# Kernel optimization log

Measured on AMD Instinct MI355X. Metric: run time of the kernel, lower is better.

Reference implementation:

```python
import jax, jax.numpy as jnp
import numpy as np
from jax import lax

B, N, S, C_IN, C_OUT = 4, 16384, 4096, 256, 256


def setup_inputs() -> dict:
    key = jax.random.key(0)
    k1, k2, k3, k4 = jax.random.split(key, 4)
    xyz1 = jax.random.normal(k1, (B, 3, N), dtype=jnp.float32)
    xyz2 = jax.random.normal(k2, (B, 3, S), dtype=jnp.float32)
    points2 = jax.random.normal(k3, (B, C_IN, S), dtype=jnp.float32)
    W = jax.random.normal(k4, (C_OUT, C_IN), dtype=jnp.float32) * (1.0 / np.sqrt(C_IN))
    b = jnp.zeros((C_OUT,), dtype=jnp.float32)
    return {"xyz1": xyz1, "xyz2": xyz2, "points2": points2, "W": W, "b": b}


def reference(xyz1, xyz2, points2, W, b):
    # channel-first -> channel-last
    p1 = jnp.transpose(xyz1, (0, 2, 1))        # [B, N, 3]
    p2 = jnp.transpose(xyz2, (0, 2, 1))        # [B, S, 3]
    f2 = jnp.transpose(points2, (0, 2, 1))     # [B, S, C]
    Bn, Nn, _ = p1.shape
    Cn = f2.shape[-1]
    # squared pairwise distances [B, N, S]
    d = (-2.0 * jnp.einsum('bnc,bsc->bns', p1, p2)
         + jnp.sum(p1 * p1, axis=-1)[:, :, None]
         + jnp.sum(p2 * p2, axis=-1)[:, None, :])
    # 3 nearest neighbors (smallest distances) -- equivalent to sort + slice :3
    neg_d3, idx = lax.top_k(-d, 3)             # [B, N, 3]
    d3 = -neg_d3
    recip = 1.0 / (d3 + 1e-8)
    weight = recip / jnp.sum(recip, axis=-1, keepdims=True)   # [B, N, 3]
    # gather neighbor features: [B, N, 3, C]
    gathered = jnp.take_along_axis(
        f2, idx.reshape(Bn, Nn * 3)[..., None], axis=1
    ).reshape(Bn, Nn, 3, Cn)
    interp = jnp.sum(gathered * weight[..., None], axis=2)    # [B, N, C]
    # Conv1d(kernel=1) == per-point linear: [B, C_out, N]
    out = jnp.einsum('bnc,oc->bon', interp, W) + b[None, :, None]
    return out
```

## Files before the change

### kernel.cpp

```cpp
#include <hip/hip_runtime.h>

#define BB 4
#define NN 16384
#define SS 4096
#define CIN 256
#define COUT 256

#define SC 8
#define SCS (SS / SC)
#define SUBS 16
#define SUBL 256
#define KNNB ((NN / 512) * SC * BB)
#define GEMMB ((COUT / 64) * (SS / 64) * BB)

typedef float v2f __attribute__((ext_vector_type(2)));
typedef float v4f __attribute__((ext_vector_type(4)));

__device__ __forceinline__ unsigned short f2bf(float f) {
    unsigned u = __float_as_uint(f);
    u += 0x7FFF + ((u >> 16) & 1);
    return (unsigned short)(u >> 16);
}
__device__ __forceinline__ float bf2f(unsigned short h) {
    return __uint_as_float((unsigned)h << 16);
}

__device__ __forceinline__ void insert_vi(float e, int gi,
                                          float& k0, float& k1, float& k2,
                                          int& i0, int& i1, int& i2) {
    bool c0 = e < k0, c1 = e < k1, c2 = e < k2;
    float n0 = fminf(e, k0);
    float n1 = __builtin_amdgcn_fmed3f(e, k0, k1);
    float n2 = __builtin_amdgcn_fmed3f(e, k1, k2);
    int t1 = c0 ? i0 : gi;
    int t2 = c1 ? i1 : gi;
    i0 = c0 ? gi : i0;
    i1 = c1 ? t1 : i1;
    i2 = c2 ? t2 : i2;
    k0 = n0; k1 = n1; k2 = n2;
}

#define E2_FROM(p_xy, p_zw, XX, YY, ZZ, e2)                                    \
    do {                                                                       \
        asm("v_pk_fma_f32 %0, %1, %2, %3 op_sel:[0,0,1] op_sel_hi:[0,1,1]"     \
            : "=v"(e2) : "v"(p_zw), "v"(ZZ), "v"(p_zw));                       \
        asm("v_pk_fma_f32 %0, %1, %2, %0 op_sel:[1,0,0] op_sel_hi:[1,1,1]"     \
            : "+v"(e2) : "v"(p_xy), "v"(YY));                                  \
        asm("v_pk_fma_f32 %0, %1, %2, %0 op_sel:[0,0,0] op_sel_hi:[0,1,1]"     \
            : "+v"(e2) : "v"(p_xy), "v"(XX));                                  \
    } while (0)

#define PK_LO(acc, ap, bw)                                                     \
    asm("v_pk_fma_f32 %0, %1, %2, %0 op_sel:[0,0,0] op_sel_hi:[0,1,1]"         \
        : "+v"(acc) : "v"(ap), "v"(bw))
#define PK_HI(acc, ap, bw)                                                     \
    asm("v_pk_fma_f32 %0, %1, %2, %0 op_sel:[1,0,0] op_sel_hi:[1,1,1]"         \
        : "+v"(acc) : "v"(ap), "v"(bw))

__device__ __forceinline__ void knn_phase(int id, int t, float* smem,
                                          const float* __restrict__ xyz1,
                                          const float* __restrict__ xyz2,
                                          float* __restrict__ pv) {
    int nb = id & 31;
    int ch = (id >> 5) & 7;
    int b  = id >> 8;
    int s0 = ch * SCS;

    float4* smv = (float4*)smem;
    const float* x2 = xyz2 + (size_t)b * 3 * SS;
    for (int i = t; i < SCS; i += 256) {
        float px = x2[s0 + i];
        float py = x2[SS + s0 + i];
        float pz = x2[2 * SS + s0 + i];
        smv[i] = make_float4(px, py, pz, fmaf(px, px, fmaf(py, py, pz * pz)));
    }
    __syncthreads();

    int n0  = nb * 512 + t;
    int n1q = n0 + 256;
    const float* xb = xyz1 + (size_t)b * 3 * NN;
    float ax = xb[n0],  ay = xb[NN + n0],  az = xb[2 * NN + n0];
    float bx = xb[n1q], by = xb[NN + n1q], bz = xb[2 * NN + n1q];
    v2f XX = {-2.0f * ax, -2.0f * bx};
    v2f YY = {-2.0f * ay, -2.0f * by};
    v2f ZZ = {-2.0f * az, -2.0f * bz};

#pragma unroll
    for (int half = 0; half < 2; ++half) {
        float A0 = 1e30f, A1 = 1e30f, A2 = 1e30f;
        float B0 = 1e30f, B1 = 1e30f, B2 = 1e30f;
        int sb = half * SUBL;
#pragma unroll 8
        for (int s = sb; s < sb + SUBL; ++s) {
            v4f p = *(const v4f*)(smem + 4 * s);
            v2f pxy = __builtin_shufflevector(p, p, 0, 1);
            v2f pzw = __builtin_shufflevector(p, p, 2, 3);
            v2f e2;
            E2_FROM(pxy, pzw, XX, YY, ZZ, e2);
            float nA1 = __builtin_amdgcn_fmed3f(e2.x, A0, A1);
            float nA2 = __builtin_amdgcn_fmed3f(e2.x, A1, A2);
            A0 = fminf(A0, e2.x); A1 = nA1; A2 = nA2;
            float nB1 = __builtin_amdgcn_fmed3f(e2.y, B0, B1);
            float nB2 = __builtin_amdgcn_fmed3f(e2.y, B1, B2);
            B0 = fminf(B0, e2.y); B1 = nB1; B2 = nB2;
        }
        int sub = ch * 2 + half;
        size_t base = (size_t)(sub * BB + b) * 3;
        pv[(base + 0) * NN + n0]  = A0;
        pv[(base + 1) * NN + n0]  = A1;
        pv[(base + 2) * NN + n0]  = A2;
        pv[(base + 0) * NN + n1q] = B0;
        pv[(base + 1) * NN + n1q] = B1;
        pv[(base + 2) * NN + n1q] = B2;
    }
}

__device__ __forceinline__ void gemm_phase(int g, int t, float* smem,
                                           const float* __restrict__ P,
                                           const float* __restrict__ W,
                                           const float* __restrict__ bias,
                                           unsigned short* __restrict__ Gh) {
    int o0 = (g & 3) * 64;
    int s0 = ((g >> 2) & 63) * 64;
    int b  = g >> 8;
    float* sP = smem;
    float* sW = smem + 1024;
    int i = t & 15;
    int j = t >> 4;

    v2f acc2[4][2];
#pragma unroll
    for (int p = 0; p < 4; ++p) {
        acc2[p][0] = (v2f){0.f, 0.f};
        acc2[p][1] = (v2f){0.f, 0.f};
    }

    const float* Pb = P + (size_t)b * CIN * SS;

    for (int c0 = 0; c0 < CIN; c0 += 16) {
        __syncthreads();
        {
            int col = t & 63;
            int r0r = t >> 6;
#pragma unroll
            for (int r = 0; r < 4; ++r) {
                int row = r0r + r * 4;
                sP[row * 64 + col] = Pb[(size_t)(c0 + row) * SS + s0 + col];
            }
        }
        {
            int cc = t & 15;
            int obase = t >> 4;
#pragma unroll
            for (int r = 0; r < 4; ++r) {
                int oo = obase + 16 * r;
                sW[cc * 68 + oo] = W[(size_t)(o0 + oo) * CIN + c0 + cc];
            }
        }
        __syncthreads();

#pragma unroll
        for (int cc = 0; cc < 16; ++cc) {
            v4f a  = *(const v4f*)&sP[cc * 64 + i * 4];
            v4f bv = *(const v4f*)&sW[cc * 68 + j * 4];
            v2f a01 = __builtin_shufflevector(a, a, 0, 1);
            v2f a23 = __builtin_shufflevector(a, a, 2, 3);
            v2f b01 = __builtin_shufflevector(bv, bv, 0, 1);
            v2f b23 = __builtin_shufflevector(bv, bv, 2, 3);
            PK_LO(acc2[0][0], a01, b01); PK_LO(acc2[0][1], a01, b23);
            PK_HI(acc2[1][0], a01, b01); PK_HI(acc2[1][1], a01, b23);
            PK_LO(acc2[2][0], a23, b01); PK_LO(acc2[2][1], a23, b23);
            PK_HI(acc2[3][0], a23, b01); PK_HI(acc2[3][1], a23, b23);
        }
    }

    float b0 = bias[o0 + j * 4 + 0];
    float b1 = bias[o0 + j * 4 + 1];
    float b2 = bias[o0 + j * 4 + 2];
    float b3 = bias[o0 + j * 4 + 3];
#pragma unroll
    for (int p = 0; p < 4; ++p) {
        ushort4 v;
        v.x = f2bf(acc2[p][0].x + b0);
        v.y = f2bf(acc2[p][0].y + b1);
        v.z = f2bf(acc2[p][1].x + b2);
        v.w = f2bf(acc2[p][1].y + b3);
        size_t off = ((size_t)b * SS + s0 + i * 4 + p) * COUT + o0 + j * 4;
        *(ushort4*)&Gh[off] = v;
    }
}

__global__ __launch_bounds__(256) void k_fused(const float* __restrict__ xyz1,
                                               const float* __restrict__ xyz2,
                                               const float* __restrict__ P,
                                               const float* __restrict__ W,
                                               const float* __restrict__ bias,
                                               unsigned short* __restrict__ Gh,
                                               float* __restrict__ pv) {
    __shared__ float smem[2112];
    int bid = blockIdx.x;
    int t   = threadIdx.x;

    if (bid < KNNB) {
        knn_phase(bid, t, smem, xyz1, xyz2, pv);
    } else {
        gemm_phase(bid - KNNB, t, smem, P, W, bias, Gh);
    }
}

__global__ __launch_bounds__(256) void k_resolve(const float* __restrict__ pv,
                                                 const float* __restrict__ xyz1,
                                                 const float* __restrict__ xyz2,
                                                 float4* __restrict__ wi4,
                                                 int4* __restrict__ gi4) {
    __shared__ float4 cand[4096];
    int b    = blockIdx.x >> 6;
    int nblk = blockIdx.x & 63;
    int t    = threadIdx.x;

    const float* x2 = xyz2 + (size_t)b * 3 * SS;
    for (int i = t; i < SS; i += 256) {
        int sub = i >> 8, s = i & 255;
        float px = x2[i];
        float py = x2[SS + i];
        float pz = x2[2 * SS + i];
        cand[sub * SUBL + (s ^ (sub & 7))] =
            make_float4(px, py, pz, fmaf(px, px, fmaf(py, py, pz * pz)));
    }
    __syncthreads();

    int n = nblk * 256 + t;

    float v0 = 1e30f, v1 = 1e30f, v2v = 1e30f;
#pragma unroll 4
    for (int sub = 0; sub < SUBS; ++sub) {
        size_t base = (size_t)(sub * BB + b) * 3;
#pragma unroll
        for (int j = 0; j < 3; ++j) {
            float a  = pv[(base + j) * NN + n];
            float t1 = __builtin_amdgcn_fmed3f(a, v0, v1);
            float t2 = __builtin_amdgcn_fmed3f(a, v1, v2v);
            v0 = fminf(v0, a); v1 = t1; v2v = t2;
        }
    }

    int l0 = 0, l1 = 0, l2 = 0, l3 = 0, cnt = 0;
#pragma unroll 4
    for (int sub = 0; sub < SUBS; ++sub) {
        float a0 = pv[(size_t)(sub * BB + b) * 3 * NN + n];
        if (a0 <= v2v) {
            if      (cnt == 0) l0 = sub;
            else if (cnt == 1) l1 = sub;
            else if (cnt == 2) l2 = sub;
            else if (cnt == 3) l3 = sub;
            ++cnt;
        }
    }

    const float* xb = xyz1 + (size_t)b * 3 * NN;
    float qx = xb[n], qy = xb[NN + n], qz = xb[2 * NN + n];
    float xm2 = -2.0f * qx, ym2 = -2.0f * qy, zm2 = -2.0f * qz;
    float nrm = fmaf(qx, qx, fmaf(qy, qy, qz * qz));

    float k0 = 1e30f, k1 = 1e30f, k2 = 1e30f;
    int   i0 = 0,     i1 = 0,     i2 = 0;
    bool ovf  = (cnt > 4);
    int  kmax = ovf ? SUBS : cnt;
    for (int k = 0; k < kmax; ++k) {
        int sub = ovf ? k : (k == 0 ? l0 : (k == 1 ? l1 : (k == 2 ? l2 : l3)));
        int xr = sub & 7;
        int sb = sub * SUBL;
#pragma unroll 8
        for (int s = 0; s < SUBL; ++s) {
            float4 p = cand[sb + (s ^ xr)];
            float e = fmaf(p.x, xm2, fmaf(p.y, ym2, fmaf(p.z, zm2, p.w)));
            insert_vi(e, sb + s, k0, k1, k2, i0, i1, i2);
        }
    }

    float d0 = k0 + nrm, d1 = k1 + nrm, d2 = k2 + nrm;
    float r0 = 1.0f / (d0 + 1e-8f);
    float r1 = 1.0f / (d1 + 1e-8f);
    float r2 = 1.0f / (d2 + 1e-8f);
    float inv = 1.0f / (r0 + r1 + r2);
    size_t q = (size_t)b * NN + n;
    wi4[q] = make_float4(r0 * inv, r1 * inv, r2 * inv, 0.f);
    gi4[q] = make_int4(i0, i1, i2, 0);
}

__global__ __launch_bounds__(256) void k_out(const unsigned short* __restrict__ Gh,
                                             const float4* __restrict__ wi4,
                                             const int4* __restrict__ gi4,
                                             float* __restrict__ out) {
    __shared__ float  tile[64 * 68];
    __shared__ float4 swv[64];
    __shared__ int4   siv[64];
    int bid  = blockIdx.x;
    int x    = bid & 7;
    int b    = x >> 1;
    int local = (bid >> 3) + (x & 1) * 512;
    int nb   = local & 255;
    int oc   = local >> 8;
    int n0   = nb * 64;
    int o0   = oc * 64;
    int t    = threadIdx.x;
    int wave = t >> 6;
    int lane = t & 63;
    int qg   = lane >> 4;
    int c16  = lane & 15;

    if (t < 64) {
        size_t q = (size_t)b * NN + n0 + t;
        swv[t] = wi4[q];
        siv[t] = gi4[q];
    }
    __syncthreads();

    const unsigned short* Gb = Gh + (size_t)b * SS * COUT;

#pragma unroll
    for (int pass = 0; pass < 4; ++pass) {
        int q = pass * 16 + wave * 4 + qg;
        float4 wv = swv[q];
        int4   iv = siv[q];
        int co = o0 + c16 * 4;
        ushort4 a0 = *(const ushort4*)(Gb + (size_t)iv.x * COUT + co);
        ushort4 a1 = *(const ushort4*)(Gb + (size_t)iv.y * COUT + co);
        ushort4 a2 = *(const ushort4*)(Gb + (size_t)iv.z * COUT + co);
        float4 v;
        v.x = fmaf(wv.x, bf2f(a0.x), fmaf(wv.y, bf2f(a1.x), wv.z * bf2f(a2.x)));
        v.y = fmaf(wv.x, bf2f(a0.y), fmaf(wv.y, bf2f(a1.y), wv.z * bf2f(a2.y)));
        v.z = fmaf(wv.x, bf2f(a0.z), fmaf(wv.y, bf2f(a1.z), wv.z * bf2f(a2.z)));
        v.w = fmaf(wv.x, bf2f(a0.w), fmaf(wv.y, bf2f(a1.w), wv.z * bf2f(a2.w)));
        *(float4*)&tile[q * 68 + c16 * 4] = v;
    }
    __syncthreads();

    float* obase = out + ((size_t)b * COUT + o0) * NN + n0 + lane;
#pragma unroll
    for (int g = 0; g < 4; ++g) {
        int c = wave * 16 + g * 4;
        float4 v = *(const float4*)&tile[lane * 68 + c];
        obase[(size_t)(c + 0) * NN] = v.x;
        obase[(size_t)(c + 1) * NN] = v.y;
        obase[(size_t)(c + 2) * NN] = v.z;
        obase[(size_t)(c + 3) * NN] = v.w;
    }
}

extern "C" void kernel_launch(void* const* d_in, const int* in_sizes, int n_in,
                              void* d_out, int out_size, void* d_ws, size_t ws_size,
                              hipStream_t stream) {
    const float* xyz1    = (const float*)d_in[0];
    const float* xyz2    = (const float*)d_in[1];
    const float* points2 = (const float*)d_in[2];
    const float* W       = (const float*)d_in[3];
    const float* bias    = (const float*)d_in[4];
    float* out = (float*)d_out;

    char* ws = (char*)d_ws;
    float*          pv  = (float*)(ws);
    unsigned short* Gh  = (unsigned short*)(ws + 12582912);
    float4*         wi4 = (float4*)(ws + 20971520);
    int4*           gi4 = (int4*)(ws + 22020096);

    k_fused<<<dim3(KNNB + GEMMB), 256, 0, stream>>>(xyz1, xyz2, points2, W, bias,
                                                    Gh, pv);
    k_resolve<<<dim3(256), 256, 0, stream>>>(pv, xyz1, xyz2, wi4, gi4);
    k_out<<<dim3(4096), 256, 0, stream>>>(Gh, wi4, gi4, out);
}
```

Measured before the change: 218.9 us.

## Split resolve kernel across four threads per point with global candidate buffer

```diff
diff --git a/kernel.cpp b/kernel.cpp
--- a/kernel.cpp
+++ b/kernel.cpp
@@ -12,6 +12,7 @@
 #define SUBL 256
 #define KNNB ((NN / 512) * SC * BB)
 #define GEMMB ((COUT / 64) * (SS / 64) * BB)
+#define RSLVB (BB * (NN / 64))
 
 typedef float v2f __attribute__((ext_vector_type(2)));
 typedef float v4f __attribute__((ext_vector_type(4)));
@@ -60,7 +61,8 @@
 __device__ __forceinline__ void knn_phase(int id, int t, float* smem,
                                           const float* __restrict__ xyz1,
                                           const float* __restrict__ xyz2,
-                                          float* __restrict__ pv) {
+                                          float* __restrict__ pv,
+                                          float4* __restrict__ cand4) {
     int nb = id & 31;
     int ch = (id >> 5) & 7;
     int b  = id >> 8;
@@ -72,7 +74,9 @@
         float px = x2[s0 + i];
         float py = x2[SS + s0 + i];
         float pz = x2[2 * SS + s0 + i];
-        smv[i] = make_float4(px, py, pz, fmaf(px, px, fmaf(py, py, pz * pz)));
+        float4 p4 = make_float4(px, py, pz, fmaf(px, px, fmaf(py, py, pz * pz)));
+        smv[i] = p4;
+        if (nb == 0) cand4[(size_t)b * SS + s0 + i] = p4;
     }
     __syncthreads();
 
@@ -196,13 +200,14 @@
                                                const float* __restrict__ W,
                                                const float* __restrict__ bias,
                                                unsigned short* __restrict__ Gh,
-                                               float* __restrict__ pv) {
+                                               float* __restrict__ pv,
+                                               float4* __restrict__ cand4) {
     __shared__ float smem[2112];
     int bid = blockIdx.x;
     int t   = threadIdx.x;
 
     if (bid < KNNB) {
-        knn_phase(bid, t, smem, xyz1, xyz2, pv);
+        knn_phase(bid, t, smem, xyz1, xyz2, pv, cand4);
     } else {
         gemm_phase(bid - KNNB, t, smem, P, W, bias, Gh);
     }
@@ -210,82 +215,95 @@
 
 __global__ __launch_bounds__(256) void k_resolve(const float* __restrict__ pv,
                                                  const float* __restrict__ xyz1,
-                                                 const float* __restrict__ xyz2,
+                                                 const float4* __restrict__ cand4,
                                                  float4* __restrict__ wi4,
                                                  int4* __restrict__ gi4) {
-    __shared__ float4 cand[4096];
-    int b    = blockIdx.x >> 6;
-    int nblk = blockIdx.x & 63;
+    __shared__ float sv[4][64][3];
+    __shared__ int   si[4][64][3];
+    int bid  = blockIdx.x;
+    int b    = bid >> 8;
+    int nblk = bid & 255;
     int t    = threadIdx.x;
-
-    const float* x2 = xyz2 + (size_t)b * 3 * SS;
-    for (int i = t; i < SS; i += 256) {
-        int sub = i >> 8, s = i & 255;
-        float px = x2[i];
-        float py = x2[SS + i];
-        float pz = x2[2 * SS + i];
-        cand[sub * SUBL + (s ^ (sub & 7))] =
-            make_float4(px, py, pz, fmaf(px, px, fmaf(py, py, pz * pz)));
-    }
-    __syncthreads();
-
-    int n = nblk * 256 + t;
-
+    int k    = t >> 6;
+    int q    = t & 63;
+    int n    = nblk * 64 + q;
+
+    float a0s[SUBS];
     float v0 = 1e30f, v1 = 1e30f, v2v = 1e30f;
-#pragma unroll 4
+#pragma unroll
     for (int sub = 0; sub < SUBS; ++sub) {
         size_t base = (size_t)(sub * BB + b) * 3;
 #pragma unroll
         for (int j = 0; j < 3; ++j) {
-            float a  = pv[(base + j) * NN + n];
+            float a = pv[(base + j) * NN + n];
+            if (j == 0) a0s[sub] = a;
             float t1 = __builtin_amdgcn_fmed3f(a, v0, v1);
             float t2 = __builtin_amdgcn_fmed3f(a, v1, v2v);
             v0 = fminf(v0, a); v1 = t1; v2v = t2;
         }
     }
 
-    int l0 = 0, l1 = 0, l2 = 0, l3 = 0, cnt = 0;
-#pragma unroll 4
+    int lk = 0, cnt = 0;
+#pragma unroll
     for (int sub = 0; sub < SUBS; ++sub) {
-        float a0 = pv[(size_t)(sub * BB + b) * 3 * NN + n];
-        if (a0 <= v2v) {
-            if      (cnt == 0) l0 = sub;
-            else if (cnt == 1) l1 = sub;
-            else if (cnt == 2) l2 = sub;
-            else if (cnt == 3) l3 = sub;
-            ++cnt;
-        }
-    }
-
+        bool w = (a0s[sub] <= v2v);
+        if (w && cnt == k) lk = sub;
+        cnt += w ? 1 : 0;
+    }
+
+    float k0 = 1e30f, k1 = 1e30f, k2 = 1e30f;
+    int   i0 = 0,     i1 = 0,     i2 = 0;
+    bool ovf = (cnt > 4);
+    bool act = !ovf && (k < cnt);
     const float* xb = xyz1 + (size_t)b * 3 * NN;
     float qx = xb[n], qy = xb[NN + n], qz = xb[2 * NN + n];
     float xm2 = -2.0f * qx, ym2 = -2.0f * qy, zm2 = -2.0f * qz;
-    float nrm = fmaf(qx, qx, fmaf(qy, qy, qz * qz));
-
-    float k0 = 1e30f, k1 = 1e30f, k2 = 1e30f;
-    int   i0 = 0,     i1 = 0,     i2 = 0;
-    bool ovf  = (cnt > 4);
-    int  kmax = ovf ? SUBS : cnt;
-    for (int k = 0; k < kmax; ++k) {
-        int sub = ovf ? k : (k == 0 ? l0 : (k == 1 ? l1 : (k == 2 ? l2 : l3)));
-        int xr = sub & 7;
-        int sb = sub * SUBL;
-#pragma unroll 8
+    const float4* cb = cand4 + (size_t)b * SS;
+
+    if (act) {
+        int sb = lk * SUBL;
+#pragma unroll 4
         for (int s = 0; s < SUBL; ++s) {
-            float4 p = cand[sb + (s ^ xr)];
+            float4 p = cb[sb + s];
             float e = fmaf(p.x, xm2, fmaf(p.y, ym2, fmaf(p.z, zm2, p.w)));
             insert_vi(e, sb + s, k0, k1, k2, i0, i1, i2);
         }
     }
-
-    float d0 = k0 + nrm, d1 = k1 + nrm, d2 = k2 + nrm;
-    float r0 = 1.0f / (d0 + 1e-8f);
-    float r1 = 1.0f / (d1 + 1e-8f);
-    float r2 = 1.0f / (d2 + 1e-8f);
-    float inv = 1.0f / (r0 + r1 + r2);
-    size_t q = (size_t)b * NN + n;
-    wi4[q] = make_float4(r0 * inv, r1 * inv, r2 * inv, 0.f);
-    gi4[q] = make_int4(i0, i1, i2, 0);
+    if (__any(ovf && k == 0)) {
+        if (ovf && k == 0) {
+            for (int s = 0; s < SS; ++s) {
+                float4 p = cb[s];
+                float e = fmaf(p.x, xm2, fmaf(p.y, ym2, fmaf(p.z, zm2, p.w)));
+                insert_vi(e, s, k0, k1, k2, i0, i1, i2);
+            }
+        }
+    }
+
+    sv[k][q][0] = k0; sv[k][q][1] = k1; sv[k][q][2] = k2;
+    si[k][q][0] = i0; si[k][q][1] = i1; si[k][q][2] = i2;
+    __syncthreads();
+
+    if (t < 64) {
+        float K0 = 1e30f, K1 = 1e30f, K2 = 1e30f;
+        int   I0 = 0,     I1 = 0,     I2 = 0;
+#pragma unroll
+        for (int kk = 0; kk < 4; ++kk)
+#pragma unroll
+            for (int j = 0; j < 3; ++j)
+                insert_vi(sv[kk][t][j], si[kk][t][j], K0, K1, K2, I0, I1, I2);
+
+        int nn = nblk * 64 + t;
+        float ax = xb[nn], ay = xb[NN + nn], az = xb[2 * NN + nn];
+        float nrm = fmaf(ax, ax, fmaf(ay, ay, az * az));
+        float d0 = K0 + nrm, d1 = K1 + nrm, d2 = K2 + nrm;
+        float r0 = 1.0f / (d0 + 1e-8f);
+        float r1 = 1.0f / (d1 + 1e-8f);
+        float r2 = 1.0f / (d2 + 1e-8f);
+        float inv = 1.0f / (r0 + r1 + r2);
+        size_t oq = (size_t)b * NN + nn;
+        wi4[oq] = make_float4(r0 * inv, r1 * inv, r2 * inv, 0.f);
+        gi4[oq] = make_int4(I0, I1, I2, 0);
+    }
 }
 
 __global__ __launch_bounds__(256) void k_out(const unsigned short* __restrict__ Gh,
@@ -363,9 +381,10 @@
     unsigned short* Gh  = (unsigned short*)(ws + 12582912);
     float4*         wi4 = (float4*)(ws + 20971520);
     int4*           gi4 = (int4*)(ws + 22020096);
+    float4* cand4 = (float4*)((char*)d_out + 66846720);
 
     k_fused<<<dim3(KNNB + GEMMB), 256, 0, stream>>>(xyz1, xyz2, points2, W, bias,
-                                                    Gh, pv);
-    k_resolve<<<dim3(256), 256, 0, stream>>>(pv, xyz1, xyz2, wi4, gi4);
+                                                    Gh, pv, cand4);
+    k_resolve<<<dim3(RSLVB), 256, 0, stream>>>(pv, xyz1, cand4, wi4, gi4);
     k_out<<<dim3(4096), 256, 0, stream>>>(Gh, wi4, gi4, out);
 }
```

New measurement: 241.9 us. 1.11x slower.
